# Performance work log

Hardware: AMD Instinct MI355X
Metric: run time of the kernel (lower is better)

Reference implementation:

```python
import math
import jax, jax.numpy as jnp
import numpy as np

NQ = 10      # n_qubits
NB = 4       # n_blocks (angle encoding layers)
VD = 6       # vqc_depth (hardware-efficient layers)
LAT = 128    # latent_dim
NOBS = 9     # n_qubits - k_local + 1 sliding 2-local groups
DIM = 2 ** NQ


def sin_embed(t, dim):
    half = dim // 2
    freqs = jnp.exp(-math.log(10000.0) * jnp.arange(half, dtype=jnp.float32) / half)
    args = t[:, None] * freqs[None, :]
    return jnp.concatenate([jnp.cos(args), jnp.sin(args)], axis=-1)


def apply_ry(psi, theta, q):
    # psi: [B, 2^NQ] complex; theta: scalar or [B]
    B = psi.shape[0]
    p = psi.reshape(B, 2 ** q, 2, 2 ** (NQ - 1 - q))
    th = jnp.broadcast_to(theta, (B,))
    c = jnp.cos(th / 2)[:, None, None].astype(psi.dtype)
    s = jnp.sin(th / 2)[:, None, None].astype(psi.dtype)
    p0, p1 = p[:, :, 0, :], p[:, :, 1, :]
    return jnp.stack([c * p0 - s * p1, s * p0 + c * p1], axis=2).reshape(B, -1)


def apply_cnot(psi, ctrl, tgt):
    B = psi.shape[0]
    pt = psi.reshape((B,) + (2,) * NQ)
    p0 = jax.lax.index_in_dim(pt, 0, axis=ctrl + 1, keepdims=True)
    p1 = jnp.flip(jax.lax.index_in_dim(pt, 1, axis=ctrl + 1, keepdims=True), axis=tgt + 1)
    return jnp.concatenate([p0, p1], axis=ctrl + 1).reshape(B, -1)


def run_circuit(enc, var_params):
    B = enc.shape[0]
    psi = jnp.zeros((B, DIM), dtype=jnp.complex64).at[:, 0].set(1.0)
    # angle encoding: RY data re-uploading blocks with CNOT ladders between blocks
    for layer in range(NB):
        for q in range(NQ):
            psi = apply_ry(psi, enc[:, layer * NQ + q], q)
        if layer < NB - 1:
            for q in range(0, NQ - 1, 2):
                psi = apply_cnot(psi, q, q + 1)
            for q in range(1, NQ - 1, 2):
                psi = apply_cnot(psi, q, q + 1)
    # hardware-efficient variational layers
    for ly in range(VD):
        for q in range(NQ):
            psi = apply_ry(psi, var_params[ly, q], q)
        for q in range(0, NQ - 1, 2):
            psi = apply_cnot(psi, q, q + 1)
        for q in range(1, NQ - 1, 2):
            psi = apply_cnot(psi, q, q + 1)
    return psi


def build_H(A_p, B_p, D_p):
    # create_Hermitian: lower-tri (row-major) = A + iB; h[i-1,i-1] = D[i]; H = h + h^dagger
    r, c = np.tril_indices(4, -1)  # order matches count+j loop: (1,0),(2,0),(2,1),(3,0),(3,1),(3,2)
    L = jnp.zeros((NOBS, 4, 4), dtype=jnp.complex64)
    L = L.at[:, r, c].set(A_p.astype(jnp.complex64) + 1j * B_p.astype(jnp.complex64))
    d = 2.0 * jnp.concatenate([D_p[:, 1:4], jnp.zeros((NOBS, 1), dtype=D_p.dtype)], axis=1)
    H = L + jnp.conj(jnp.swapaxes(L, 1, 2))
    H = H + jax.vmap(jnp.diag)(d).astype(jnp.complex64)
    return H


def expvals(psi, H):
    B = psi.shape[0]
    outs = []
    for s in range(NOBS):  # sliding window [s, s+1]
        pg = psi.reshape(B, 2 ** s, 4, 2 ** (NQ - s - 2))
        outs.append(jnp.einsum('balr,lk,bakr->b', jnp.conj(pg), H[s], pg).real)
    return jnp.stack(outs, axis=-1)


def setup_inputs() -> dict:
    ks = jax.random.split(jax.random.key(0), 12)
    B = 2048
    return {
        'z_t': jax.random.normal(ks[0], (B, LAT), dtype=jnp.float32),
        't': jax.random.uniform(ks[1], (B,), dtype=jnp.float32),
        'W1': 0.05 * jax.random.normal(ks[2], (2 * LAT, 256), dtype=jnp.float32),
        'b1': jnp.zeros((256,), dtype=jnp.float32),
        'W2': 0.05 * jax.random.normal(ks[3], (256, NB * NQ), dtype=jnp.float32),
        'b2': jnp.zeros((NB * NQ,), dtype=jnp.float32),
        'var_params': 0.01 * jax.random.normal(ks[4], (VD, NQ), dtype=jnp.float32),
        'A_p': 2.0 * jax.random.normal(ks[5], (NOBS, 6), dtype=jnp.float32),
        'B_p': 2.0 * jax.random.normal(ks[6], (NOBS, 6), dtype=jnp.float32),
        'D_p': 2.0 * jax.random.normal(ks[7], (NOBS, 4), dtype=jnp.float32),
        'W3': 0.05 * jax.random.normal(ks[8], (NOBS, 256), dtype=jnp.float32),
        'b3': jnp.zeros((256,), dtype=jnp.float32),
        'W4': 0.05 * jax.random.normal(ks[9], (256, LAT), dtype=jnp.float32),
        'b4': jnp.zeros((LAT,), dtype=jnp.float32),
    }


def reference(z_t, t, W1, b1, W2, b2, var_params, A_p, B_p, D_p, W3, b3, W4, b4):
    x = jnp.concatenate([z_t, sin_embed(t, LAT)], axis=-1)   # [B, 2*LAT]
    h = jax.nn.silu(x @ W1 + b1)
    enc = h @ W2 + b2                                         # [B, NB*NQ]
    psi = run_circuit(enc, var_params)                        # [B, 2^NQ]
    obs = expvals(psi, build_H(A_p, B_p, D_p))                # [B, NOBS]
    return jax.nn.silu(obs @ W3 + b3) @ W4 + b4               # [B, LAT]
```

## Files before the change

kernel.cpp:

```cpp
#include <hip/hip_runtime.h>
#include <math.h>

#define NOBS 9
#define LATD 128

typedef unsigned u32x2 __attribute__((ext_vector_type(2)));

__device__ __forceinline__ float silu_f(float x) { return x / (1.f + expf(-x)); }


template<int CTRL>
__device__ __forceinline__ float dpp_perm(float x) {
  return __int_as_float(__builtin_amdgcn_update_dpp(0, __float_as_int(x), CTRL, 0xF, 0xF, true));
}
template<int PAT>
__device__ __forceinline__ float ds_swz(float x) {
  return __int_as_float(__builtin_amdgcn_ds_swizzle(__float_as_int(x), PAT));
}

__device__ __forceinline__ float x4(float x) { return ds_swz<0x101F>(x); }

#if __has_builtin(__builtin_amdgcn_permlane32_swap)
#define PL32 1
__device__ __forceinline__ float x32(float x, bool sel) {
  u32x2 r = __builtin_amdgcn_permlane32_swap(__float_as_uint(x), __float_as_uint(x), false, false);
  return __uint_as_float(sel ? r.x : r.y);
}
__device__ __forceinline__ float sum32(float x) {
  u32x2 r = __builtin_amdgcn_permlane32_swap(__float_as_uint(x), __float_as_uint(x), false, false);
  return __uint_as_float(r.x) + __uint_as_float(r.y);
}
#else
#define PL32 0
__device__ __forceinline__ float x32(float x, bool sel) { return __shfl_xor(x, 32, 64); }
__device__ __forceinline__ float sum32(float x) { return x + __shfl_xor(x, 32, 64); }
#endif

#if __has_builtin(__builtin_amdgcn_permlane16_swap)
#define PL16 1
__device__ __forceinline__ float x16(float x, bool sel) {
  u32x2 r = __builtin_amdgcn_permlane16_swap(__float_as_uint(x), __float_as_uint(x), false, false);
  return __uint_as_float(sel ? r.x : r.y);
}
__device__ __forceinline__ float sum16(float x) {
  u32x2 r = __builtin_amdgcn_permlane16_swap(__float_as_uint(x), __float_as_uint(x), false, false);
  return __uint_as_float(r.x) + __uint_as_float(r.y);
}
#else
#define PL16 0
__device__ __forceinline__ float x16(float x, bool sel) { return ds_swz<0x401F>(x); }
__device__ __forceinline__ float sum16(float x) { return x + ds_swz<0x401F>(x); }
#endif

__device__ __forceinline__ float wave_sum(float x) {
  x += dpp_perm<0xB1>(x);
  x += dpp_perm<0x4E>(x);
  x += x4(x);
  x += dpp_perm<0x128>(x);
  x = sum16(x);
  x = sum32(x);
  return x;
}


template<int M>
__device__ __forceinline__ void ry_reg(float v[16], float c, float s) {
#pragma unroll
  for (int r = 0; r < 16; ++r) {
    if ((r & M) == 0) {
      float p0 = v[r], p1 = v[r | M];
      v[r]     = c * p0 - s * p1;
      v[r | M] = s * p0 + c * p1;
    }
  }
}

__device__ __forceinline__ void apply_rys(float v[16], int lane, bool sel32, bool sel16,
                                          const float* __restrict__ cc,
                                          const float* __restrict__ ss) {
  ry_reg<8>(v, cc[0], ss[0]);
  ry_reg<4>(v, cc[1], ss[1]);
  ry_reg<2>(v, cc[2], ss[2]);
  ry_reg<1>(v, cc[3], ss[3]);
  { float c = cc[4], s = ss[4], sp = (lane & 32) ? s : -s;
#pragma unroll
    for (int r = 0; r < 16; ++r) { float p = x32(v[r], sel32); v[r] = fmaf(c, v[r], sp * p); } }
  { float c = cc[5], s = ss[5], sp = (lane & 16) ? s : -s;
#pragma unroll
    for (int r = 0; r < 16; ++r) { float p = x16(v[r], sel16); v[r] = fmaf(c, v[r], sp * p); } }
  { float c = cc[6], s = ss[6], sp = (lane & 8) ? s : -s;
#pragma unroll
    for (int r = 0; r < 16; ++r) { float p = dpp_perm<0x128>(v[r]); v[r] = fmaf(c, v[r], sp * p); } }
  { float c = cc[7], s = ss[7], sp = (lane & 4) ? s : -s;
#pragma unroll
    for (int r = 0; r < 16; ++r) { float p = x4(v[r]); v[r] = fmaf(c, v[r], sp * p); } }
  { float c = cc[8], s = ss[8], sp = (lane & 2) ? s : -s;
#pragma unroll
    for (int r = 0; r < 16; ++r) { float p = dpp_perm<0x4E>(v[r]); v[r] = fmaf(c, v[r], sp * p); } }
  { float c = cc[9], s = ss[9], sp = (lane & 1) ? s : -s;
#pragma unroll
    for (int r = 0; r < 16; ++r) { float p = dpp_perm<0xB1>(v[r]); v[r] = fmaf(c, v[r], sp * p); } }
}

__device__ __forceinline__ void cnot_ladder(float v[16], int lane, bool sel32, bool sel16) {
  float t;
  t=v[8];  v[8]=v[12];  v[12]=t;
  t=v[9];  v[9]=v[13];  v[13]=t;
  t=v[10]; v[10]=v[14]; v[14]=t;
  t=v[11]; v[11]=v[15]; v[15]=t;
  t=v[2];  v[2]=v[3];   v[3]=t;
  t=v[6];  v[6]=v[7];   v[7]=t;
  t=v[10]; v[10]=v[11]; v[11]=t;
  t=v[14]; v[14]=v[15]; v[15]=t;
  { bool c45 = (lane & 32);
#pragma unroll
    for (int r = 0; r < 16; ++r) { float p = x16(v[r], sel16); v[r] = c45 ? p : v[r]; } }
  { bool c67 = (lane & 8);
#pragma unroll
    for (int r = 0; r < 16; ++r) { float p = x4(v[r]); v[r] = c67 ? p : v[r]; } }
  { bool c89 = (lane & 2);
#pragma unroll
    for (int r = 0; r < 16; ++r) { float p = dpp_perm<0xB1>(v[r]); v[r] = c89 ? p : v[r]; } }
  t=v[4];  v[4]=v[6];   v[6]=t;
  t=v[5];  v[5]=v[7];   v[7]=t;
  t=v[12]; v[12]=v[14]; v[14]=t;
  t=v[13]; v[13]=v[15]; v[15]=t;
#pragma unroll
  for (int r = 1; r < 16; r += 2) v[r] = x32(v[r], sel32);
  { bool c56 = (lane & 16);
#pragma unroll
    for (int r = 0; r < 16; ++r) { float p = dpp_perm<0x128>(v[r]); v[r] = c56 ? p : v[r]; } }
  { bool c78 = (lane & 4);
#pragma unroll
    for (int r = 0; r < 16; ++r) { float p = dpp_perm<0x4E>(v[r]); v[r] = c78 ? p : v[r]; } }
}


__global__ __launch_bounds__(128) void fused_kernel(
    const float* __restrict__ z, const float* __restrict__ t,
    const float* __restrict__ W1, const float* __restrict__ b1,
    const float* __restrict__ W2, const float* __restrict__ b2,
    const float* __restrict__ varp,
    const float* __restrict__ A_p, const float* __restrict__ D_p,
    const float* __restrict__ W3, const float* __restrict__ b3,
    const float* __restrict__ W4, const float* __restrict__ b4,
    float* __restrict__ out) {
  __shared__ float xs[2][256];
  __shared__ float hs[2][256];
  __shared__ float dump[2][1024];
  __shared__ float cs[2][40], sn[2][40];
  __shared__ float vcs[60], vsn[60];
  __shared__ float os[2][NOBS];

  int tid = threadIdx.x;
  int b0 = blockIdx.x * 2;

  if (tid < 60) {
    float s, c;
    sincosf(0.5f * varp[tid], &s, &c);
    vcs[tid] = c; vsn[tid] = s;
  }

  {
    int j = tid & 63;
    float freq = expf(-9.2103403719761836f * (float)j * (1.f / 64.f));
#pragma unroll
    for (int r = 0; r < 2; ++r) {
      int b = b0 + r;
      xs[r][tid] = z[b * 128 + tid];
      float arg = t[b] * freq;
      xs[r][tid + 128] = (tid < 64) ? cosf(arg) : sinf(arg);
    }
  }
  __syncthreads();

  {
    float a00 = b1[tid],       a10 = a00;
    float a01 = b1[tid + 128], a11 = a01;
#pragma unroll 4
    for (int k = 0; k < 256; k += 4) {
      float w00 = W1[(k + 0) * 256 + tid], w01 = W1[(k + 0) * 256 + tid + 128];
      float w10 = W1[(k + 1) * 256 + tid], w11 = W1[(k + 1) * 256 + tid + 128];
      float w20 = W1[(k + 2) * 256 + tid], w21 = W1[(k + 2) * 256 + tid + 128];
      float w30 = W1[(k + 3) * 256 + tid], w31 = W1[(k + 3) * 256 + tid + 128];
      float4 x0 = *(const float4*)&xs[0][k];
      float4 x1 = *(const float4*)&xs[1][k];
      a00 = fmaf(x0.w, w30, fmaf(x0.z, w20, fmaf(x0.y, w10, fmaf(x0.x, w00, a00))));
      a01 = fmaf(x0.w, w31, fmaf(x0.z, w21, fmaf(x0.y, w11, fmaf(x0.x, w01, a01))));
      a10 = fmaf(x1.w, w30, fmaf(x1.z, w20, fmaf(x1.y, w10, fmaf(x1.x, w00, a10))));
      a11 = fmaf(x1.w, w31, fmaf(x1.z, w21, fmaf(x1.y, w11, fmaf(x1.x, w01, a11))));
    }
    hs[0][tid]       = silu_f(a00);
    hs[0][tid + 128] = silu_f(a01);
    hs[1][tid]       = silu_f(a10);
    hs[1][tid + 128] = silu_f(a11);
  }
  __syncthreads();

  if (tid < 80) {
    int r = tid / 40, c = tid - r * 40;
    float acc = b2[c];
#pragma unroll 4
    for (int k = 0; k < 256; k += 4) {
      float4 h = *(const float4*)&hs[r][k];
      acc = fmaf(h.x, W2[(k + 0) * 40 + c], acc);
      acc = fmaf(h.y, W2[(k + 1) * 40 + c], acc);
      acc = fmaf(h.z, W2[(k + 2) * 40 + c], acc);
      acc = fmaf(h.w, W2[(k + 3) * 40 + c], acc);
    }
    float s, cv;
    sincosf(0.5f * acc, &s, &cv);
    cs[r][c] = cv; sn[r][c] = s;
  }
  __syncthreads();

  {
    int wave = tid >> 6;
    int lane = tid & 63;
    bool sel32 = true, sel16 = true;
#if PL32
    { u32x2 tt = __builtin_amdgcn_permlane32_swap((unsigned)lane, (unsigned)lane, false, false);
      sel32 = (tt.x == (unsigned)(lane ^ 32)); }
#endif
#if PL16
    { u32x2 tt = __builtin_amdgcn_permlane16_swap((unsigned)lane, (unsigned)lane, false, false);
      sel16 = (tt.x == (unsigned)(lane ^ 16)); }
#endif
    const float* cc = cs[wave];
    const float* ss = sn[wave];

    float base = 1.f;
    base *= (lane & 32) ? ss[4] : cc[4];
    base *= (lane & 16) ? ss[5] : cc[5];
    base *= (lane & 8)  ? ss[6] : cc[6];
    base *= (lane & 4)  ? ss[7] : cc[7];
    base *= (lane & 2)  ? ss[8] : cc[8];
    base *= (lane & 1)  ? ss[9] : cc[9];
    float v[16];
#pragma unroll
    for (int r = 0; r < 16; ++r) {
      float p = base;
      p *= (r & 8) ? ss[0] : cc[0];
      p *= (r & 4) ? ss[1] : cc[1];
      p *= (r & 2) ? ss[2] : cc[2];
      p *= (r & 1) ? ss[3] : cc[3];
      v[r] = p;
    }
    cnot_ladder(v, lane, sel32, sel16);
#pragma unroll 1
    for (int layer = 1; layer < 4; ++layer) {
      apply_rys(v, lane, sel32, sel16, cc + layer * 10, ss + layer * 10);
      if (layer < 3) cnot_ladder(v, lane, sel32, sel16);
    }
#pragma unroll 1
    for (int ly = 0; ly < 6; ++ly) {
      apply_rys(v, lane, sel32, sel16, vcs + ly * 10, vsn + ly * 10);
      cnot_ladder(v, lane, sel32, sel16);
    }

    float* sw = dump[wave];
#pragma unroll
    for (int r = 0; r < 16; ++r) sw[r * 64 + lane] = v[r];

#pragma unroll 1
    for (int s = 0; s < NOBS; ++s) {
      const int r8 = 8 - s;
      const int stride = 1 << r8;
      float h10 = A_p[s*6+0], h20 = A_p[s*6+1], h21 = A_p[s*6+2];
      float h30 = A_p[s*6+3], h31 = A_p[s*6+4], h32 = A_p[s*6+5];
      float d0 = 2.f * D_p[s*4+1], d1 = 2.f * D_p[s*4+2], d2 = 2.f * D_p[s*4+3];
      float acc = 0.f;
#pragma unroll
      for (int k = 0; k < 4; ++k) {
        int p = lane + 64 * k;
        int a  = p >> r8;
        int rr = p & (stride - 1);
        int bse = (a << (r8 + 2)) + rr;
        float x0 = sw[bse];
        float x1 = sw[bse + stride];
        float x2 = sw[bse + 2 * stride];
        float x3 = sw[bse + 3 * stride];
        acc += d0 * x0 * x0 + d1 * x1 * x1 + d2 * x2 * x2
             + 2.f * (h10 * x1 * x0 + h20 * x2 * x0 + h21 * x2 * x1
                    + h30 * x3 * x0 + h31 * x3 * x1 + h32 * x3 * x2);
      }
      acc = wave_sum(acc);
      if (lane == 0) os[wave][s] = acc;
    }
  }
  __syncthreads();

  {
    float a00 = b3[tid],       a10 = a00;
    float a01 = b3[tid + 128], a11 = a01;
#pragma unroll
    for (int s = 0; s < NOBS; ++s) {
      float w0 = W3[s * 256 + tid];
      float w1 = W3[s * 256 + tid + 128];
      float o0 = os[0][s], o1 = os[1][s];
      a00 = fmaf(o0, w0, a00);
      a01 = fmaf(o0, w1, a01);
      a10 = fmaf(o1, w0, a10);
      a11 = fmaf(o1, w1, a11);
    }
    hs[0][tid]       = silu_f(a00);
    hs[0][tid + 128] = silu_f(a01);
    hs[1][tid]       = silu_f(a10);
    hs[1][tid + 128] = silu_f(a11);
  }
  __syncthreads();
  {
    int c = tid;
    float o0 = b4[c], o1 = o0;
#pragma unroll 4
    for (int k = 0; k < 256; k += 4) {
      float w0 = W4[(k + 0) * 128 + c];
      float w1 = W4[(k + 1) * 128 + c];
      float w2 = W4[(k + 2) * 128 + c];
      float w3 = W4[(k + 3) * 128 + c];
      float4 ha = *(const float4*)&hs[0][k];
      float4 hb = *(const float4*)&hs[1][k];
      o0 = fmaf(ha.w, w3, fmaf(ha.z, w2, fmaf(ha.y, w1, fmaf(ha.x, w0, o0))));
      o1 = fmaf(hb.w, w3, fmaf(hb.z, w2, fmaf(hb.y, w1, fmaf(hb.x, w0, o1))));
    }
    out[(b0 + 0) * LATD + c] = o0;
    out[(b0 + 1) * LATD + c] = o1;
  }
}


extern "C" void kernel_launch(void* const* d_in, const int* in_sizes, int n_in,
                              void* d_out, int out_size, void* d_ws, size_t ws_size,
                              hipStream_t stream) {
  const float* z_t  = (const float*)d_in[0];
  const float* t    = (const float*)d_in[1];
  const float* W1   = (const float*)d_in[2];
  const float* b1   = (const float*)d_in[3];
  const float* W2   = (const float*)d_in[4];
  const float* b2   = (const float*)d_in[5];
  const float* varp = (const float*)d_in[6];
  const float* A_p  = (const float*)d_in[7];
  const float* D_p  = (const float*)d_in[9];
  const float* W3   = (const float*)d_in[10];
  const float* b3   = (const float*)d_in[11];
  const float* W4   = (const float*)d_in[12];
  const float* b4   = (const float*)d_in[13];
  float* out = (float*)d_out;

  int B = in_sizes[1];

  fused_kernel<<<B / 2, 128, 0, stream>>>(z_t, t, W1, b1, W2, b2, varp,
                                          A_p, D_p, W3, b3, W4, b4, out);
}
```

Measured before the change: 132.7 us.

## Process eight samples per block with LDS-staged double-buffered weight tiles

Each block now handles 8 batch rows with 512 threads instead of 2 rows with 128. The W1, W2 and W4 weights are streamed through shared memory in double-buffered float4 tiles, with register prefetch of the next tile. The dense layers use packed float2 FMAs across row pairs. The aim is to cut redundant global weight traffic per sample and to overlap loads with compute. The cost is more barriers, a larger LDS footprint that limits occupancy, and fewer blocks in flight.

```diff
diff --git a/kernel.cpp b/kernel.cpp
--- a/kernel.cpp
+++ b/kernel.cpp
@@ -2,11 +2,13 @@
 #include <math.h>
 
 #define NOBS 9
-#define LATD 128
-
+
+typedef float f2 __attribute__((ext_vector_type(2)));
 typedef unsigned u32x2 __attribute__((ext_vector_type(2)));
 
 __device__ __forceinline__ float silu_f(float x) { return x / (1.f + expf(-x)); }
+__device__ __forceinline__ f2 splat2(float x) { return (f2){x, x}; }
+__device__ __forceinline__ f2 fma2(f2 a, f2 b, f2 c) { return __builtin_elementwise_fma(a, b, c); }
 
 
 template<int CTRL>
@@ -17,8 +19,7 @@
 __device__ __forceinline__ float ds_swz(float x) {
   return __int_as_float(__builtin_amdgcn_ds_swizzle(__float_as_int(x), PAT));
 }
-
-__device__ __forceinline__ float x4(float x) { return ds_swz<0x101F>(x); }
+__device__ __forceinline__ float x4f(float x) { return ds_swz<0x101F>(x); }
 
 #if __has_builtin(__builtin_amdgcn_permlane32_swap)
 #define PL32 1
@@ -55,7 +56,7 @@
 __device__ __forceinline__ float wave_sum(float x) {
   x += dpp_perm<0xB1>(x);
   x += dpp_perm<0x4E>(x);
-  x += x4(x);
+  x += x4f(x);
   x += dpp_perm<0x128>(x);
   x = sum16(x);
   x = sum32(x);
@@ -93,7 +94,7 @@
     for (int r = 0; r < 16; ++r) { float p = dpp_perm<0x128>(v[r]); v[r] = fmaf(c, v[r], sp * p); } }
   { float c = cc[7], s = ss[7], sp = (lane & 4) ? s : -s;
 #pragma unroll
-    for (int r = 0; r < 16; ++r) { float p = x4(v[r]); v[r] = fmaf(c, v[r], sp * p); } }
+    for (int r = 0; r < 16; ++r) { float p = x4f(v[r]); v[r] = fmaf(c, v[r], sp * p); } }
   { float c = cc[8], s = ss[8], sp = (lane & 2) ? s : -s;
 #pragma unroll
     for (int r = 0; r < 16; ++r) { float p = dpp_perm<0x4E>(v[r]); v[r] = fmaf(c, v[r], sp * p); } }
@@ -117,7 +118,7 @@
     for (int r = 0; r < 16; ++r) { float p = x16(v[r], sel16); v[r] = c45 ? p : v[r]; } }
   { bool c67 = (lane & 8);
 #pragma unroll
-    for (int r = 0; r < 16; ++r) { float p = x4(v[r]); v[r] = c67 ? p : v[r]; } }
+    for (int r = 0; r < 16; ++r) { float p = x4f(v[r]); v[r] = c67 ? p : v[r]; } }
   { bool c89 = (lane & 2);
 #pragma unroll
     for (int r = 0; r < 16; ++r) { float p = dpp_perm<0xB1>(v[r]); v[r] = c89 ? p : v[r]; } }
@@ -136,7 +137,7 @@
 }
 
 
-__global__ __launch_bounds__(128) void fused_kernel(
+__global__ __launch_bounds__(512) void fused_kernel(
     const float* __restrict__ z, const float* __restrict__ t,
     const float* __restrict__ W1, const float* __restrict__ b1,
     const float* __restrict__ W2, const float* __restrict__ b2,
@@ -145,89 +146,137 @@
     const float* __restrict__ W3, const float* __restrict__ b3,
     const float* __restrict__ W4, const float* __restrict__ b4,
     float* __restrict__ out) {
-  __shared__ float xs[2][256];
-  __shared__ float hs[2][256];
-  __shared__ float dump[2][1024];
-  __shared__ float cs[2][40], sn[2][40];
-  __shared__ float vcs[60], vsn[60];
-  __shared__ float os[2][NOBS];
-
-  int tid = threadIdx.x;
-  int b0 = blockIdx.x * 2;
+  __shared__ __align__(16) float lds[15176];
+  f2*    xs2 = (f2*)(lds + 8192);
+  f2*    hs2 = (f2*)(lds + 10240);
+  f2*    hp2 = (f2*)(lds + 12288);
+  float* hsf = lds + 10240;
+  float* cs_ = lds + 14336;
+  float* sn_ = lds + 14656;
+  float* vcs = lds + 14976;
+  float* vsn = lds + 15040;
+  float* osb = lds + 15104;
+
+  const int tid  = threadIdx.x;
+  const int b0   = blockIdx.x * 8;
+  const int col  = tid & 255;
+  const int half = tid >> 8;
+  const int lane = tid & 63;
+  const int wave = tid >> 6;
+
+  const float4* gW1 = (const float4*)W1;
+  const float4* gW2 = (const float4*)W2;
+  const float4* gW4 = (const float4*)W4;
+
+  float4 pre0 = gW1[tid], pre1 = gW1[512 + tid];
+  __builtin_amdgcn_sched_barrier(0);
 
   if (tid < 60) {
     float s, c;
     sincosf(0.5f * varp[tid], &s, &c);
     vcs[tid] = c; vsn[tid] = s;
   }
-
-  {
-    int j = tid & 63;
-    float freq = expf(-9.2103403719761836f * (float)j * (1.f / 64.f));
-#pragma unroll
-    for (int r = 0; r < 2; ++r) {
-      int b = b0 + r;
-      xs[r][tid] = z[b * 128 + tid];
-      float arg = t[b] * freq;
-      xs[r][tid + 128] = (tid < 64) ? cosf(arg) : sinf(arg);
-    }
-  }
+  {
+    int k = tid & 255, ph = tid >> 8;
+#pragma unroll
+    for (int q = 0; q < 2; ++q) {
+      int rp = 2 * ph + q;
+      if (k < 128) {
+        xs2[rp * 256 + k] = (f2){z[(b0 + 2 * rp) * 128 + k], z[(b0 + 2 * rp + 1) * 128 + k]};
+      } else {
+        int i = k - 128, j = i & 63;
+        float freq = expf(-9.2103403719761836f * (float)j * (1.f / 64.f));
+        float a0 = t[b0 + 2 * rp] * freq, a1 = t[b0 + 2 * rp + 1] * freq;
+        xs2[rp * 256 + k] = (i < 64) ? (f2){cosf(a0), cosf(a1)} : (f2){sinf(a0), sinf(a1)};
+      }
+    }
+  }
+  { float4* d = (float4*)lds; d[tid] = pre0; d[512 + tid] = pre1; }
   __syncthreads();
 
   {
-    float a00 = b1[tid],       a10 = a00;
-    float a01 = b1[tid + 128], a11 = a01;
+    f2 acc0 = splat2(b1[col]), acc1 = acc0;
+    const int rp0 = 2 * half, rp1 = rp0 + 1;
+#pragma unroll 1
+    for (int tt = 0; tt < 16; ++tt) {
+      if (tt < 15) {
+        pre0 = gW1[(tt + 1) * 1024 + tid];
+        pre1 = gW1[(tt + 1) * 1024 + 512 + tid];
+        __builtin_amdgcn_sched_barrier(0);
+      }
+      const float* wt = lds + (tt & 1) * 4096;
+#pragma unroll
+      for (int kk = 0; kk < 16; ++kk) {
+        float wv = wt[kk * 256 + col];
+        int k = tt * 16 + kk;
+        acc0 = fma2(xs2[rp0 * 256 + k], splat2(wv), acc0);
+        acc1 = fma2(xs2[rp1 * 256 + k], splat2(wv), acc1);
+      }
+      if (tt < 15) {
+        float4* d = (float4*)(lds + ((tt + 1) & 1) * 4096);
+        d[tid] = pre0; d[512 + tid] = pre1;
+      }
+      __syncthreads();
+    }
+    hs2[rp0 * 256 + col] = (f2){silu_f(acc0.x), silu_f(acc0.y)};
+    hs2[rp1 * 256 + col] = (f2){silu_f(acc1.x), silu_f(acc1.y)};
+  }
+
+  float p3acc = 0.f;
+  const int p3r = tid / 40, p3c = tid - p3r * 40;
+  {
+    float4 pa0 = gW2[tid], pa1 = gW2[512 + tid], pa2;
+    if (tid < 256) pa2 = gW2[1024 + tid];
+    __builtin_amdgcn_sched_barrier(0);
+    {
+      float4* d = (float4*)lds;
+      d[tid] = pa0; d[512 + tid] = pa1; if (tid < 256) d[1024 + tid] = pa2;
+    }
+    __syncthreads();
+
+    float4 pb0 = gW2[1280 + tid], pb1 = gW2[1792 + tid], pb2;
+    if (tid < 256) pb2 = gW2[2304 + tid];
+    __builtin_amdgcn_sched_barrier(0);
+    if (tid < 320) {
+      float a = b2[p3c];
 #pragma unroll 4
-    for (int k = 0; k < 256; k += 4) {
-      float w00 = W1[(k + 0) * 256 + tid], w01 = W1[(k + 0) * 256 + tid + 128];
-      float w10 = W1[(k + 1) * 256 + tid], w11 = W1[(k + 1) * 256 + tid + 128];
-      float w20 = W1[(k + 2) * 256 + tid], w21 = W1[(k + 2) * 256 + tid + 128];
-      float w30 = W1[(k + 3) * 256 + tid], w31 = W1[(k + 3) * 256 + tid + 128];
-      float4 x0 = *(const float4*)&xs[0][k];
-      float4 x1 = *(const float4*)&xs[1][k];
-      a00 = fmaf(x0.w, w30, fmaf(x0.z, w20, fmaf(x0.y, w10, fmaf(x0.x, w00, a00))));
-      a01 = fmaf(x0.w, w31, fmaf(x0.z, w21, fmaf(x0.y, w11, fmaf(x0.x, w01, a01))));
-      a10 = fmaf(x1.w, w30, fmaf(x1.z, w20, fmaf(x1.y, w10, fmaf(x1.x, w00, a10))));
-      a11 = fmaf(x1.w, w31, fmaf(x1.z, w21, fmaf(x1.y, w11, fmaf(x1.x, w01, a11))));
-    }
-    hs[0][tid]       = silu_f(a00);
-    hs[0][tid + 128] = silu_f(a01);
-    hs[1][tid]       = silu_f(a10);
-    hs[1][tid + 128] = silu_f(a11);
+      for (int k = 0; k < 128; ++k)
+        a = fmaf(hsf[(p3r >> 1) * 512 + 2 * k + (p3r & 1)], lds[k * 40 + p3c], a);
+      p3acc = a;
+    }
+    __syncthreads();
+    {
+      float4* d = (float4*)lds;
+      d[tid] = pb0; d[512 + tid] = pb1; if (tid < 256) d[1024 + tid] = pb2;
+    }
+    __syncthreads();
+    if (tid < 320) {
+      float a = p3acc;
+#pragma unroll 4
+      for (int k = 0; k < 128; ++k)
+        a = fmaf(hsf[(p3r >> 1) * 512 + 2 * (128 + k) + (p3r & 1)], lds[k * 40 + p3c], a);
+      float s, cv;
+      sincosf(0.5f * a, &s, &cv);
+      cs_[p3r * 40 + p3c] = cv;
+      sn_[p3r * 40 + p3c] = s;
+    }
   }
   __syncthreads();
 
-  if (tid < 80) {
-    int r = tid / 40, c = tid - r * 40;
-    float acc = b2[c];
-#pragma unroll 4
-    for (int k = 0; k < 256; k += 4) {
-      float4 h = *(const float4*)&hs[r][k];
-      acc = fmaf(h.x, W2[(k + 0) * 40 + c], acc);
-      acc = fmaf(h.y, W2[(k + 1) * 40 + c], acc);
-      acc = fmaf(h.z, W2[(k + 2) * 40 + c], acc);
-      acc = fmaf(h.w, W2[(k + 3) * 40 + c], acc);
-    }
-    float s, cv;
-    sincosf(0.5f * acc, &s, &cv);
-    cs[r][c] = cv; sn[r][c] = s;
-  }
-  __syncthreads();
-
-  {
-    int wave = tid >> 6;
-    int lane = tid & 63;
+  float4 w4p0 = gW4[tid], w4p1 = gW4[512 + tid];
+  __builtin_amdgcn_sched_barrier(0);
+  {
     bool sel32 = true, sel16 = true;
 #if PL32
-    { u32x2 tt = __builtin_amdgcn_permlane32_swap((unsigned)lane, (unsigned)lane, false, false);
-      sel32 = (tt.x == (unsigned)(lane ^ 32)); }
+    { u32x2 tt2 = __builtin_amdgcn_permlane32_swap((unsigned)lane, (unsigned)lane, false, false);
+      sel32 = (tt2.x == (unsigned)(lane ^ 32)); }
 #endif
 #if PL16
-    { u32x2 tt = __builtin_amdgcn_permlane16_swap((unsigned)lane, (unsigned)lane, false, false);
-      sel16 = (tt.x == (unsigned)(lane ^ 16)); }
+    { u32x2 tt2 = __builtin_amdgcn_permlane16_swap((unsigned)lane, (unsigned)lane, false, false);
+      sel16 = (tt2.x == (unsigned)(lane ^ 16)); }
 #endif
-    const float* cc = cs[wave];
-    const float* ss = sn[wave];
+    const float* cc = cs_ + wave * 40;
+    const float* ss = sn_ + wave * 40;
 
     float base = 1.f;
     base *= (lane & 32) ? ss[4] : cc[4];
@@ -258,7 +307,7 @@
       cnot_ladder(v, lane, sel32, sel16);
     }
 
-    float* sw = dump[wave];
+    float* sw = lds + wave * 1024;
 #pragma unroll
     for (int r = 0; r < 16; ++r) sw[r * 64 + lane] = v[r];
 
@@ -285,46 +334,50 @@
                     + h30 * x3 * x0 + h31 * x3 * x1 + h32 * x3 * x2);
       }
       acc = wave_sum(acc);
-      if (lane == 0) os[wave][s] = acc;
+      if (lane == 0) osb[wave * 9 + s] = acc;
     }
   }
   __syncthreads();
 
-  {
-    float a00 = b3[tid],       a10 = a00;
-    float a01 = b3[tid + 128], a11 = a01;
+  { float4* d = (float4*)lds; d[tid] = w4p0; d[512 + tid] = w4p1; }
+  {
+    f2 a0 = splat2(b3[col]), a1 = a0;
 #pragma unroll
     for (int s = 0; s < NOBS; ++s) {
-      float w0 = W3[s * 256 + tid];
-      float w1 = W3[s * 256 + tid + 128];
-      float o0 = os[0][s], o1 = os[1][s];
-      a00 = fmaf(o0, w0, a00);
-      a01 = fmaf(o0, w1, a01);
-      a10 = fmaf(o1, w0, a10);
-      a11 = fmaf(o1, w1, a11);
-    }
-    hs[0][tid]       = silu_f(a00);
-    hs[0][tid + 128] = silu_f(a01);
-    hs[1][tid]       = silu_f(a10);
-    hs[1][tid + 128] = silu_f(a11);
+      float wv = W3[s * 256 + col];
+      a0 = fma2((f2){osb[(4 * half + 0) * 9 + s], osb[(4 * half + 1) * 9 + s]}, splat2(wv), a0);
+      a1 = fma2((f2){osb[(4 * half + 2) * 9 + s], osb[(4 * half + 3) * 9 + s]}, splat2(wv), a1);
+    }
+    hp2[(2 * half) * 256 + col]     = (f2){silu_f(a0.x), silu_f(a0.y)};
+    hp2[(2 * half + 1) * 256 + col] = (f2){silu_f(a1.x), silu_f(a1.y)};
   }
   __syncthreads();
-  {
-    int c = tid;
-    float o0 = b4[c], o1 = o0;
-#pragma unroll 4
-    for (int k = 0; k < 256; k += 4) {
-      float w0 = W4[(k + 0) * 128 + c];
-      float w1 = W4[(k + 1) * 128 + c];
-      float w2 = W4[(k + 2) * 128 + c];
-      float w3 = W4[(k + 3) * 128 + c];
-      float4 ha = *(const float4*)&hs[0][k];
-      float4 hb = *(const float4*)&hs[1][k];
-      o0 = fmaf(ha.w, w3, fmaf(ha.z, w2, fmaf(ha.y, w1, fmaf(ha.x, w0, o0))));
-      o1 = fmaf(hb.w, w3, fmaf(hb.z, w2, fmaf(hb.y, w1, fmaf(hb.x, w0, o1))));
-    }
-    out[(b0 + 0) * LATD + c] = o0;
-    out[(b0 + 1) * LATD + c] = o1;
+
+  {
+    const int c4 = tid & 127, rq = tid >> 7;
+    f2 acc = splat2(b4[c4]);
+#pragma unroll 1
+    for (int tt = 0; tt < 8; ++tt) {
+      if (tt < 7) {
+        w4p0 = gW4[(tt + 1) * 1024 + tid];
+        w4p1 = gW4[(tt + 1) * 1024 + 512 + tid];
+        __builtin_amdgcn_sched_barrier(0);
+      }
+      const float* wt = lds + (tt & 1) * 4096;
+#pragma unroll
+      for (int kk = 0; kk < 32; ++kk) {
+        float wv = wt[kk * 128 + c4];
+        int k = tt * 32 + kk;
+        acc = fma2(hp2[rq * 256 + k], splat2(wv), acc);
+      }
+      if (tt < 7) {
+        float4* d = (float4*)(lds + ((tt + 1) & 1) * 4096);
+        d[tid] = w4p0; d[512 + tid] = w4p1;
+      }
+      __syncthreads();
+    }
+    out[(b0 + 2 * rq) * 128 + c4]     = acc.x;
+    out[(b0 + 2 * rq + 1) * 128 + c4] = acc.y;
   }
 }
 
@@ -349,6 +402,6 @@
 
   int B = in_sizes[1];
 
-  fused_kernel<<<B / 2, 128, 0, stream>>>(z_t, t, W1, b1, W2, b2, varp,
+  fused_kernel<<<B / 8, 512, 0, stream>>>(z_t, t, W1, b1, W2, b2, varp,
                                           A_p, D_p, W3, b3, W4, b4, out);
 }
```

Measured after the change: 133.0 us. Within noise of the previous version (+0.2%).
